# Performance work log

Measured on AMD Instinct MI355X. Metric: run time of the kernel, lower is better.

The kernel has to match this reference:

```python
import jax, jax.numpy as jnp
import numpy as np


def _conv3(x, w):
    # 3x3 conv, stride 1, padding 1 (SAME), NCHW/OIHW
    return jax.lax.conv_general_dilated(
        x, w, window_strides=(1, 1), padding=((1, 1), (1, 1)),
        dimension_numbers=("NCHW", "OIHW", "NCHW"))


def setup_inputs() -> dict:
    key = jax.random.key(0)
    ks = jax.random.split(key, 10)
    B, C, H, W = 16, 64, 128, 128
    NL = 4
    inp = {
        "x0": jax.random.normal(ks[0], (B, C, H, W), dtype=jnp.float32),
        "spa_mask": jax.random.uniform(ks[1], (B, 1, H, W), dtype=jnp.float32),
        # uniform noise in (0,1) for gumbel; bounded away from 0 like the torch retry loop
        "gumbels": jax.random.uniform(ks[2], (1, C, NL, 2), dtype=jnp.float32,
                                      minval=1e-6, maxval=1.0 - 1e-6),
        "ch_mask_param": jax.random.uniform(ks[3], (1, C, NL, 2), dtype=jnp.float32),
        "w0": jax.random.normal(ks[4], (C, C, 3, 3), dtype=jnp.float32) * 0.05,
        "w1": jax.random.normal(ks[5], (C, C, 3, 3), dtype=jnp.float32) * 0.05,
        "w2": jax.random.normal(ks[6], (C, C, 3, 3), dtype=jnp.float32) * 0.05,
        "w3": jax.random.normal(ks[7], (C, C, 3, 3), dtype=jnp.float32) * 0.05,
        "wc": jax.random.normal(ks[8], (C, C * NL, 1, 1), dtype=jnp.float32) * 0.05,
        "bc": jax.random.normal(ks[9], (C,), dtype=jnp.float32) * 0.05,
    }
    return inp


def reference(x0, spa_mask, gumbels, ch_mask_param, w0, w1, w2, w3, wc, bc):
    tau = 1.0
    g = -jnp.log(-jnp.log(gumbels))
    ch_mask = jax.nn.softmax((ch_mask_param + g) / tau, axis=3)  # (1,C,NL,2)
    ws = [w0, w1, w2, w3]
    outs = []
    fea = x0
    for i in range(4):
        m_d = ch_mask[:, :, i, 0][:, :, None, None]  # dense-path channel gate (1,C,1,1)
        m_s = ch_mask[:, :, i, 1][:, :, None, None]  # sparse-path channel gate
        if i == 0:
            fea = _conv3(fea, ws[0])
            fea = fea * m_s * spa_mask + fea * m_d
        else:
            fea_d = _conv3(fea * m_d, ws[i])
            fea_s = _conv3(fea * m_s, ws[i])
            fea = (fea_d * m_s * spa_mask + fea_d * m_d
                   + fea_s * m_s * spa_mask + fea_s * m_d * spa_mask)
        fea = jax.nn.relu(fea)
        outs.append(fea)
    cat = jnp.concatenate(outs, axis=1)  # (B, 4C, H, W)
    out = jnp.einsum("oc,bchw->bohw", wc[:, :, 0, 0], cat) + bc[None, :, None, None]
    return (out, ch_mask)
```

## Files before the change

kernel.cpp:

```cpp
#include <hip/hip_runtime.h>
#include <math.h>

#define B_ 16
#define C_ 64
#define H_ 128
#define W_ 128
#define HW_ (H_*W_)
#define OUT_ELEMS 16777216

#define CHM_B    0
#define PWA_B    2048
#define AH_B     34816
#define FEA_B(s) (550912u + (size_t)(s)*33554432u)

#define A_S0   0
#define A_S(s) (36864 + ((s)-1)*73728)

#define SUBT 14040

typedef __attribute__((ext_vector_type(4))) short  v4s;
typedef __attribute__((ext_vector_type(8))) short  v8s;
typedef __attribute__((ext_vector_type(4))) float  v4f;

__device__ __forceinline__ ushort f2bf(float f) {
    unsigned u = __builtin_bit_cast(unsigned, f);
    unsigned r = u + 0x7FFFu + ((u >> 16) & 1u);
    return (ushort)(r >> 16);
}

__global__ __launch_bounds__(64) void mask_kernel(
    const float* __restrict__ gum, const float* __restrict__ par,
    float* __restrict__ chm, float* __restrict__ out_tail)
{
    int c = threadIdx.x;
    #pragma unroll
    for (int i = 0; i < 4; ++i) {
        int base = (c*4 + i)*2;
        float g0 = -logf(-logf(gum[base]));
        float g1 = -logf(-logf(gum[base+1]));
        float a0 = par[base] + g0, a1 = par[base+1] + g1;
        float mx = fmaxf(a0, a1);
        float e0 = expf(a0 - mx), e1 = expf(a1 - mx);
        float inv = 1.0f / (e0 + e1);
        float m0 = e0*inv, m1 = e1*inv;
        chm[base] = m0; chm[base+1] = m1;
        out_tail[base] = m0; out_tail[base+1] = m1;
    }
}

__global__ __launch_bounds__(256) void prep_kernel(
    const float* __restrict__ w0, const float* __restrict__ w1,
    const float* __restrict__ w2, const float* __restrict__ w3,
    const float* __restrict__ wc, const float* __restrict__ chm,
    ushort* __restrict__ AH, ushort* __restrict__ pwA)
{
    int idx = blockIdx.x*256 + threadIdx.x;
    if (idx < 36864) {
        int blk = idx >> 11;
        int r3  = idx & 2047;
        int oc = r3 >> 5, icl = r3 & 31;
        int cc = blk / 9, t = blk - 9*cc;
        int ic = cc*32 + icl;
        AH[idx] = f2bf(w0[(oc*64 + ic)*9 + t]);
    } else if (idx < 258048) {
        int j = idx - 36864;
        int s = 1 + j / 73728;
        int r = j % 73728;
        int blk = r >> 12;
        int r3  = r & 4095;
        int ocM = r3 >> 5, icl = r3 & 31;
        int cc = blk / 9, t = blk - 9*cc;
        int ic = cc*32 + icl;
        int oc = ocM >> 1, set = ocM & 1;
        const float* wsrc = (s == 1) ? w1 : (s == 2 ? w2 : w3);
        AH[idx] = f2bf(wsrc[(oc*64 + ic)*9 + t] * chm[(ic*4 + s)*2 + set]);
    } else {
        int r = idx - 258048;
        pwA[r] = f2bf(wc[r]);
    }
}

template<int NSETS, bool INF32>
__global__ __launch_bounds__(256, 2) void conv_bf16(
    const void* __restrict__ inv, const ushort* __restrict__ A,
    const float* __restrict__ chm, const float* __restrict__ spa,
    ushort* __restrict__ feaOut, int stage)
{
    constexpr int MOC = 64*NSETS;
    constexpr int MT  = MOC/32;
    __shared__ __align__(16) ushort sB[2*SUBT];

    const int tid  = threadIdx.x;
    const int lane = tid & 63, wave = tid >> 6;
    const int wrow = wave >> 1, wcol = wave & 1;
    const int q = lane >> 4, ln16 = lane & 15;
    const int wk = (blockIdx.x & 7)*256 + (blockIdx.x >> 3);
    const int h = wk & 127, b = wk >> 7;

    v4f acc[MT][4];
    #pragma unroll
    for (int m = 0; m < MT; ++m)
        #pragma unroll
        for (int n = 0; n < 4; ++n) acc[m][n] = (v4f){0.f, 0.f, 0.f, 0.f};

    int aRow[MT];
    #pragma unroll
    for (int m = 0; m < MT; ++m)
        aRow[m] = (wrow*(MOC/2) + m*16 + ln16)*32 + q*8;

    v8s stg[12];
    v4f stgF[24];
    v8s af[4][MT];

    auto issue = [&](int c) {
        const int ic0 = c*32;
        #pragma unroll
        for (int it = 0; it < 6; ++it) {
            int i  = it*256 + tid;
            int ry = i >> 9;
            int r  = i & 511;
            int ic = r >> 4, wv = r & 15;
            int gh = h - 1 + ry;
            if constexpr (INF32) {
                v4f a0 = (v4f){0.f,0.f,0.f,0.f}, a1 = a0;
                if ((unsigned)gh < 128u) {
                    const float* s = (const float*)inv +
                        ((size_t)((b*C_ + ic0 + ic)*H_ + gh)*W_ + wv*8);
                    a0 = *(const v4f*)(const void*)s;
                    a1 = *(const v4f*)(const void*)(s + 4);
                }
                stgF[(c*6+it)*2] = a0; stgF[(c*6+it)*2+1] = a1;
            } else {
                v8s v = (v8s){0,0,0,0,0,0,0,0};
                if ((unsigned)gh < 128u)
                    v = *(const v8s*)(const void*)((const ushort*)inv +
                        ((size_t)((b*C_ + ic0 + ic)*H_ + gh)*W_ + wv*8));
                stg[c*6+it] = v;
            }
        }
    };
    auto scatter = [&](int c) {
        ushort* sBc = sB + c*SUBT;
        #pragma unroll
        for (int it = 0; it < 6; ++it) {
            int i  = it*256 + tid;
            int ry = i >> 9;
            int r  = i & 511;
            int ic = r >> 4, wv = r & 15;
            int colBase = ry*130 + wv*8 + 1;
            ushort vals[8];
            if constexpr (INF32) {
                #pragma unroll
                for (int j = 0; j < 4; ++j) {
                    vals[j]   = f2bf(stgF[(c*6+it)*2][j]);
                    vals[4+j] = f2bf(stgF[(c*6+it)*2+1][j]);
                }
            } else {
                #pragma unroll
                for (int j = 0; j < 8; ++j) vals[j] = (ushort)stg[c*6+it][j];
            }
            #pragma unroll
            for (int j = 0; j < 8; ++j) {
                int colIdx = colBase + j;
                int s3 = (colIdx >> 3) & 7;
                sBc[colIdx*36 + (ic ^ (s3 << 2))] = vals[j];
            }
        }
    };
    auto prolog = [&]() {
        #pragma unroll
        for (int tp = 0; tp < 3; ++tp)
            #pragma unroll
            for (int m = 0; m < MT; ++m)
                af[tp][m] = *(const v8s*)(const void*)(A + tp*MOC*32 + aRow[m]);
    };
    auto loadB = [&](int tt, v8s* dst) {
        const int c  = tt/9, t = tt - 9*c;
        const int ky = t/3, kx = t - 3*(t/3);
        const ushort* sBc = sB + c*SUBT;
        #pragma unroll
        for (int nt = 0; nt < 4; ++nt) {
            int colIdx = ky*130 + wcol*64 + nt*16 + ln16 + kx;
            int s3 = (colIdx >> 3) & 7;
            int base = colIdx*36 + ((q ^ (s3 >> 1)) << 3);
            int lo = base + ((s3 & 1) << 2);
            int hi = base + (((s3 & 1) ^ 1) << 2);
            v4s va = *(const v4s*)(const void*)(sBc + lo);
            v4s vb = *(const v4s*)(const void*)(sBc + hi);
            dst[nt] = __builtin_shufflevector(va, vb, 0, 1, 2, 3, 4, 5, 6, 7);
        }
    };

    issue(0);
    issue(1);
    prolog();
    if (tid < 216) {
        int colSel = tid / 36;
        int icz    = tid - colSel*36;
        int ry     = colSel >> 1;
        int colIdx = ry*130 + ((colSel & 1) ? 129 : 0);
        sB[colIdx*36 + icz] = 0;
        sB[SUBT + colIdx*36 + icz] = 0;
    }
    scatter(0);
    scatter(1);
    __syncthreads();

    v8s bf[3][4];
    loadB(0, bf[0]);
    loadB(1, bf[1]);
    #pragma unroll
    for (int tt = 0; tt < 18; ++tt) {
        if (tt < 16) loadB(tt+2, bf[(tt+2)%3]);
        if (tt < 15) {
            #pragma unroll
            for (int m = 0; m < MT; ++m)
                af[(tt+3)&3][m] = *(const v8s*)(const void*)(A + (tt+3)*MOC*32 + aRow[m]);
        }
        #pragma unroll
        for (int nt = 0; nt < 4; ++nt)
            #pragma unroll
            for (int m = 0; m < MT; ++m)
                acc[m][nt] = __builtin_amdgcn_mfma_f32_16x16x32_bf16(af[tt&3][m], bf[tt%3][nt], acc[m][nt], 0, 0, 0);
    }

    const float* spaRow = &spa[b*HW_ + h*W_];
    #pragma unroll
    for (int nt = 0; nt < 4; ++nt) {
        int px = wcol*64 + nt*16 + ln16;
        float sp = spaRow[px];
        #pragma unroll
        for (int m = 0; m < MT; ++m) {
            if constexpr (NSETS == 2) {
                #pragma unroll
                for (int rp = 0; rp < 2; ++rp) {
                    int oc = wrow*32 + m*8 + q*2 + rp;
                    float md = chm[(oc*4 + stage)*2 + 0];
                    float ms = chm[(oc*4 + stage)*2 + 1];
                    float f = acc[m][nt][2*rp]*(ms*sp + md)
                            + acc[m][nt][2*rp+1]*((ms + md)*sp);
                    feaOut[((size_t)(b*C_ + oc)*H_ + h)*W_ + px] = f2bf(fmaxf(f, 0.f));
                }
            } else {
                #pragma unroll
                for (int r = 0; r < 4; ++r) {
                    int oc = wrow*32 + m*16 + q*4 + r;
                    float md = chm[(oc*4 + stage)*2 + 0];
                    float ms = chm[(oc*4 + stage)*2 + 1];
                    float f = acc[m][nt][r]*(ms*sp + md);
                    feaOut[((size_t)(b*C_ + oc)*H_ + h)*W_ + px] = f2bf(fmaxf(f, 0.f));
                }
            }
        }
    }
}

__global__ __launch_bounds__(256, 2) void pw_final(
    const ushort* __restrict__ fea, const ushort* __restrict__ pwA,
    const float* __restrict__ bc, float* __restrict__ out)
{
    __shared__ __align__(16) ushort sF[64*260];

    const int tid  = threadIdx.x;
    const int lane = tid & 63, wave = tid >> 6;
    const int wrow = wave >> 1, wcol = wave & 1;
    const int q = lane >> 4, ln16 = lane & 15;
    const int half = blockIdx.x & 1;
    const int h = (blockIdx.x >> 1) & 127;
    const int b = blockIdx.x >> 8;
    const int px0 = half*64;

    {
        v8s stg[8];
        #pragma unroll
        for (int it = 0; it < 8; ++it) {
            int i  = it*256 + tid;
            int s  = i >> 9;
            int r  = i & 511;
            int ic = r >> 3, pxv = r & 7;
            stg[it] = *(const v8s*)(const void*)(
                fea + (size_t)s*OUT_ELEMS + ((size_t)(b*C_ + ic)*H_ + h)*W_ + px0 + pxv*8);
        }
        #pragma unroll
        for (int it = 0; it < 8; ++it) {
            int i  = it*256 + tid;
            int s  = i >> 9;
            int r  = i & 511;
            int ic = r >> 3, pxv = r & 7;
            int kS = (s*64 + ic) ^ ((pxv & 3) << 3);
            ushort* dst = &sF[(pxv*8)*260 + kS];
            #pragma unroll
            for (int j = 0; j < 8; ++j) dst[j*260] = (ushort)stg[it][j];
        }
    }
    __syncthreads();

    v4f acc[2][2];
    #pragma unroll
    for (int m = 0; m < 2; ++m)
        #pragma unroll
        for (int n = 0; n < 2; ++n) acc[m][n] = (v4f){0.f, 0.f, 0.f, 0.f};

    #pragma unroll
    for (int ks = 0; ks < 8; ++ks) {
        v8s a[2];
        #pragma unroll
        for (int m = 0; m < 2; ++m)
            a[m] = *(const v8s*)(const void*)(pwA + (wrow*32 + m*16 + ln16)*256 + ks*32 + q*8);
        #pragma unroll
        for (int n = 0; n < 2; ++n) {
            int px = wcol*32 + n*16 + ln16;
            int swz = (px >> 3) & 3;
            v4s va = *(const v4s*)(const void*)(sF + px*260 + ks*32 + ((q ^ swz) << 3));
            v4s vb = *(const v4s*)(const void*)(sF + px*260 + ks*32 + ((q ^ swz) << 3) + 4);
            v8s bf = __builtin_shufflevector(va, vb, 0, 1, 2, 3, 4, 5, 6, 7);
            #pragma unroll
            for (int m = 0; m < 2; ++m)
                acc[m][n] = __builtin_amdgcn_mfma_f32_16x16x32_bf16(a[m], bf, acc[m][n], 0, 0, 0);
        }
    }

    #pragma unroll
    for (int n = 0; n < 2; ++n) {
        int px = px0 + wcol*32 + n*16 + ln16;
        #pragma unroll
        for (int m = 0; m < 2; ++m)
            #pragma unroll
            for (int r = 0; r < 4; ++r) {
                int o = wrow*32 + m*16 + q*4 + r;
                out[((size_t)(b*C_ + o)*H_ + h)*W_ + px] = acc[m][n][r] + bc[o];
            }
    }
}

extern "C" void kernel_launch(void* const* d_in, const int* in_sizes, int n_in,
                              void* d_out, int out_size, void* d_ws, size_t ws_size,
                              hipStream_t stream)
{
    const float* x0  = (const float*)d_in[0];
    const float* spa = (const float*)d_in[1];
    const float* gum = (const float*)d_in[2];
    const float* par = (const float*)d_in[3];
    const float* w0  = (const float*)d_in[4];
    const float* w1  = (const float*)d_in[5];
    const float* w2  = (const float*)d_in[6];
    const float* w3  = (const float*)d_in[7];
    const float* wc  = (const float*)d_in[8];
    const float* bc  = (const float*)d_in[9];
    float* out = (float*)d_out;
    char*  ws  = (char*)d_ws;

    float*  chm = (float*)(ws + CHM_B);
    ushort* pwA = (ushort*)(ws + PWA_B);
    ushort* AH  = (ushort*)(ws + AH_B);
    ushort* fea0 = (ushort*)(ws + FEA_B(0));
    ushort* fea1 = (ushort*)(ws + FEA_B(1));
    ushort* fea2 = (ushort*)(ws + FEA_B(2));
    ushort* fea3 = (ushort*)(ws + FEA_B(3));

    mask_kernel<<<1, 64, 0, stream>>>(gum, par, chm, out + OUT_ELEMS);
    prep_kernel<<<1072, 256, 0, stream>>>(w0, w1, w2, w3, wc, chm, AH, pwA);

    conv_bf16<1, true ><<<2048, 256, 0, stream>>>(x0,   AH + A_S0,  chm, spa, fea0, 0);
    conv_bf16<2, false><<<2048, 256, 0, stream>>>(fea0, AH + A_S(1), chm, spa, fea1, 1);
    conv_bf16<2, false><<<2048, 256, 0, stream>>>(fea1, AH + A_S(2), chm, spa, fea2, 2);
    conv_bf16<2, false><<<2048, 256, 0, stream>>>(fea2, AH + A_S(3), chm, spa, fea3, 3);

    pw_final<<<4096, 256, 0, stream>>>(fea0, pwA, bc, out);
}
```

Measured before the change: 378.5 us.

## Store intermediate features channels-last and add NHWC conv kernel for stages 1-3

Intermediate bf16 feature maps are now written in NHWC layout, so each pixel's 64 channels are contiguous. A new conv_nhwc kernel loads three padded input rows into shared memory with XOR swizzling and reads 16-byte vector B fragments directly, replacing the NCHW-based conv for stages 1-3. pw_final is adapted to read NHWC features with vector LDS stores, removing the old scalar transposing scatter. The epilogue stores are now strided by 64 channels per pixel (2-byte scattered writes), which may hurt store coalescing. The change also relies on the weight layout produced by prep_kernel matching the new A indexing.

```diff
diff --git a/kernel.cpp b/kernel.cpp
--- a/kernel.cpp
+++ b/kernel.cpp
@@ -225,6 +225,7 @@
     }
 
     const float* spaRow = &spa[b*HW_ + h*W_];
+    const size_t rowBase = ((size_t)(b*H_ + h))*W_;
     #pragma unroll
     for (int nt = 0; nt < 4; ++nt) {
         int px = wcol*64 + nt*16 + ln16;
@@ -239,7 +240,7 @@
                     float ms = chm[(oc*4 + stage)*2 + 1];
                     float f = acc[m][nt][2*rp]*(ms*sp + md)
                             + acc[m][nt][2*rp+1]*((ms + md)*sp);
-                    feaOut[((size_t)(b*C_ + oc)*H_ + h)*W_ + px] = f2bf(fmaxf(f, 0.f));
+                    feaOut[(rowBase + px)*64 + oc] = f2bf(fmaxf(f, 0.f));
                 }
             } else {
                 #pragma unroll
@@ -248,8 +249,123 @@
                     float md = chm[(oc*4 + stage)*2 + 0];
                     float ms = chm[(oc*4 + stage)*2 + 1];
                     float f = acc[m][nt][r]*(ms*sp + md);
-                    feaOut[((size_t)(b*C_ + oc)*H_ + h)*W_ + px] = f2bf(fmaxf(f, 0.f));
+                    feaOut[(rowBase + px)*64 + oc] = f2bf(fmaxf(f, 0.f));
                 }
+            }
+        }
+    }
+}
+
+__global__ __launch_bounds__(256, 2) void conv_nhwc(
+    const ushort* __restrict__ fin, const ushort* __restrict__ A,
+    const float* __restrict__ chm, const float* __restrict__ spa,
+    ushort* __restrict__ feaOut, int stage)
+{
+    __shared__ __align__(16) ushort sB[3*130*64];
+
+    const int tid  = threadIdx.x;
+    const int lane = tid & 63, wave = tid >> 6;
+    const int wrow = wave >> 1, wcol = wave & 1;
+    const int q = lane >> 4, ln16 = lane & 15;
+    const int wk = (blockIdx.x & 7)*256 + (blockIdx.x >> 3);
+    const int h = wk & 127, b = wk >> 7;
+    const size_t rowBase = ((size_t)(b*H_ + h))*W_;
+
+    v4f acc[4][4];
+    #pragma unroll
+    for (int m = 0; m < 4; ++m)
+        #pragma unroll
+        for (int n = 0; n < 4; ++n) acc[m][n] = (v4f){0.f, 0.f, 0.f, 0.f};
+
+    int aRow[4];
+    #pragma unroll
+    for (int m = 0; m < 4; ++m)
+        aRow[m] = (wrow*64 + m*16 + ln16)*32 + q*8;
+
+    v8s stg[12];
+    #pragma unroll
+    for (int it = 0; it < 12; ++it) {
+        int i   = it*256 + tid;
+        int ry  = i >> 10;
+        int r   = i & 1023;
+        int col = r >> 3, grp = r & 7;
+        int gh  = h - 1 + ry;
+        v8s v = (v8s){0,0,0,0,0,0,0,0};
+        if ((unsigned)gh < 128u) {
+            int icg = grp ^ ((col + 1) & 7);
+            v = *(const v8s*)(const void*)(fin +
+                (((size_t)(b*H_ + gh))*W_ + col)*64 + icg*8);
+        }
+        stg[it] = v;
+    }
+    if (tid < 48) {
+        int ry = tid >> 4, k = tid & 15;
+        int colIdx = (k & 8) ? 129 : 0;
+        int grp = k & 7;
+        *(v8s*)(void*)(sB + (ry*130 + colIdx)*64 + grp*8) = (v8s){0,0,0,0,0,0,0,0};
+    }
+    #pragma unroll
+    for (int it = 0; it < 12; ++it) {
+        int i   = it*256 + tid;
+        int ry  = i >> 10;
+        int r   = i & 1023;
+        int col = r >> 3, grp = r & 7;
+        *(v8s*)(void*)(sB + (ry*130 + col + 1)*64 + grp*8) = stg[it];
+    }
+    __syncthreads();
+
+    v8s af[2][2][4];
+    #pragma unroll
+    for (int kk = 0; kk < 2; ++kk)
+        #pragma unroll
+        for (int m = 0; m < 4; ++m)
+            af[0][kk][m] = *(const v8s*)(const void*)(A + (size_t)(kk*9 + 0)*4096 + aRow[m]);
+
+    #pragma unroll
+    for (int t = 0; t < 9; ++t) {
+        if (t < 8) {
+            #pragma unroll
+            for (int kk = 0; kk < 2; ++kk)
+                #pragma unroll
+                for (int m = 0; m < 4; ++m)
+                    af[(t+1)&1][kk][m] = *(const v8s*)(const void*)(A + (size_t)(kk*9 + t+1)*4096 + aRow[m]);
+        }
+        const int ky = t/3, kx = t - 3*(t/3);
+        v8s bf[2][4];
+        #pragma unroll
+        for (int nt = 0; nt < 4; ++nt) {
+            int col2 = wcol*64 + nt*16 + ln16 + kx;
+            int key  = col2 & 7;
+            #pragma unroll
+            for (int kk = 0; kk < 2; ++kk) {
+                int grp = (kk*4 + q) ^ key;
+                bf[kk][nt] = *(const v8s*)(const void*)(sB + (ky*130 + col2)*64 + grp*8);
+            }
+        }
+        #pragma unroll
+        for (int nt = 0; nt < 4; ++nt)
+            #pragma unroll
+            for (int kk = 0; kk < 2; ++kk)
+                #pragma unroll
+                for (int m = 0; m < 4; ++m)
+                    acc[m][nt] = __builtin_amdgcn_mfma_f32_16x16x32_bf16(af[t&1][kk][m], bf[kk][nt], acc[m][nt], 0, 0, 0);
+    }
+
+    const float* spaRow = &spa[b*HW_ + h*W_];
+    #pragma unroll
+    for (int nt = 0; nt < 4; ++nt) {
+        int px = wcol*64 + nt*16 + ln16;
+        float sp = spaRow[px];
+        #pragma unroll
+        for (int m = 0; m < 4; ++m) {
+            #pragma unroll
+            for (int rp = 0; rp < 2; ++rp) {
+                int oc = wrow*32 + m*8 + q*2 + rp;
+                float md = chm[(oc*4 + stage)*2 + 0];
+                float ms = chm[(oc*4 + stage)*2 + 1];
+                float f = acc[m][nt][2*rp]*(ms*sp + md)
+                        + acc[m][nt][2*rp+1]*((ms + md)*sp);
+                feaOut[(rowBase + px)*64 + oc] = f2bf(fmaxf(f, 0.f));
             }
         }
     }
@@ -259,7 +375,7 @@
     const ushort* __restrict__ fea, const ushort* __restrict__ pwA,
     const float* __restrict__ bc, float* __restrict__ out)
 {
-    __shared__ __align__(16) ushort sF[64*260];
+    __shared__ __align__(16) ushort sF[4*64*64];
 
     const int tid  = threadIdx.x;
     const int lane = tid & 63, wave = tid >> 6;
@@ -277,20 +393,19 @@
             int i  = it*256 + tid;
             int s  = i >> 9;
             int r  = i & 511;
-            int ic = r >> 3, pxv = r & 7;
+            int px = r >> 3, grp = r & 7;
+            int icg = grp ^ (px & 7);
             stg[it] = *(const v8s*)(const void*)(
-                fea + (size_t)s*OUT_ELEMS + ((size_t)(b*C_ + ic)*H_ + h)*W_ + px0 + pxv*8);
+                fea + (size_t)s*OUT_ELEMS +
+                (((size_t)(b*H_ + h))*W_ + px0 + px)*64 + icg*8);
         }
         #pragma unroll
         for (int it = 0; it < 8; ++it) {
             int i  = it*256 + tid;
             int s  = i >> 9;
             int r  = i & 511;
-            int ic = r >> 3, pxv = r & 7;
-            int kS = (s*64 + ic) ^ ((pxv & 3) << 3);
-            ushort* dst = &sF[(pxv*8)*260 + kS];
-            #pragma unroll
-            for (int j = 0; j < 8; ++j) dst[j*260] = (ushort)stg[it][j];
+            int px = r >> 3, grp = r & 7;
+            *(v8s*)(void*)(sF + (s*64 + px)*64 + grp*8) = stg[it];
         }
     }
     __syncthreads();
@@ -310,10 +425,9 @@
         #pragma unroll
         for (int n = 0; n < 2; ++n) {
             int px = wcol*32 + n*16 + ln16;
-            int swz = (px >> 3) & 3;
-            v4s va = *(const v4s*)(const void*)(sF + px*260 + ks*32 + ((q ^ swz) << 3));
-            v4s vb = *(const v4s*)(const void*)(sF + px*260 + ks*32 + ((q ^ swz) << 3) + 4);
-            v8s bf = __builtin_shufflevector(va, vb, 0, 1, 2, 3, 4, 5, 6, 7);
+            int s  = ks >> 1;
+            int grp = ((ks & 1)*4 + q) ^ (px & 7);
+            v8s bf = *(const v8s*)(const void*)(sF + (s*64 + px)*64 + grp*8);
             #pragma unroll
             for (int m = 0; m < 2; ++m)
                 acc[m][n] = __builtin_amdgcn_mfma_f32_16x16x32_bf16(a[m], bf, acc[m][n], 0, 0, 0);
@@ -361,10 +475,10 @@
     mask_kernel<<<1, 64, 0, stream>>>(gum, par, chm, out + OUT_ELEMS);
     prep_kernel<<<1072, 256, 0, stream>>>(w0, w1, w2, w3, wc, chm, AH, pwA);
 
-    conv_bf16<1, true ><<<2048, 256, 0, stream>>>(x0,   AH + A_S0,  chm, spa, fea0, 0);
-    conv_bf16<2, false><<<2048, 256, 0, stream>>>(fea0, AH + A_S(1), chm, spa, fea1, 1);
-    conv_bf16<2, false><<<2048, 256, 0, stream>>>(fea1, AH + A_S(2), chm, spa, fea2, 2);
-    conv_bf16<2, false><<<2048, 256, 0, stream>>>(fea2, AH + A_S(3), chm, spa, fea3, 3);
+    conv_bf16<1, true><<<2048, 256, 0, stream>>>(x0, AH + A_S0, chm, spa, fea0, 0);
+    conv_nhwc<<<2048, 256, 0, stream>>>(fea0, AH + A_S(1), chm, spa, fea1, 1);
+    conv_nhwc<<<2048, 256, 0, stream>>>(fea1, AH + A_S(2), chm, spa, fea2, 2);
+    conv_nhwc<<<2048, 256, 0, stream>>>(fea2, AH + A_S(3), chm, spa, fea3, 3);
 
     pw_final<<<4096, 256, 0, stream>>>(fea0, pwA, bc, out);
 }
```

After: 408.9 us. +8.0%, slower.
